# Performance work log

Hardware: AMD Instinct MI355X
Metric: run time of the kernel (lower is better)

The kernel has to match this reference:

```python
import jax, jax.numpy as jnp
import numpy as np

B, H, S, D = 2, 16, 2048, 64
NEG_BIG = -1e12


def setup_inputs() -> dict:
    key = jax.random.key(0)
    k1, k2, k3, k4 = jax.random.split(key, 4)
    query = jax.random.normal(k1, (B, H, S, D), dtype=jnp.float32)
    key_t = jax.random.normal(k2, (B, H, D, S), dtype=jnp.float32)  # pre-transposed key
    value = jax.random.normal(k3, (B, H, S, D), dtype=jnp.float32)
    mask = jax.random.randint(k4, (B, S), 0, 2, dtype=jnp.int32)
    return {"query": query, "key": key_t, "value": value, "mask": mask}


def reference(query, key, value, mask):
    # scores: [B,H,S,S] = query @ key (key already [B,H,D,S]) scaled by 1/sqrt(D)
    scale = 1.0 / np.sqrt(float(query.shape[-1]))
    scores = jnp.einsum('bhsd,bhdt->bhst', query, key) * scale
    # additive mask along the QUERY dimension, broadcast over keys: (B,1,S,1)
    addr = ((1.0 - mask.astype(scores.dtype)) * NEG_BIG).reshape(query.shape[0], 1, query.shape[2], 1)
    scores = scores + addr
    p_attn = jax.nn.softmax(scores, axis=-1)
    return jnp.einsum('bhst,bhtd->bhsd', p_attn, value)
```

## Files before the change

### kernel.cpp

```cpp
#include <hip/hip_runtime.h>
#include <hip/hip_bf16.h>

#define BB 2
#define HH 16
#define SLEN 2048
#define DD 64
#define QB 128
#define KB 64
#define NW 8
#define NT (SLEN / KB)
#define NBH (BB * HH)
#define LOG2E 1.44269504088896340736f

typedef __attribute__((ext_vector_type(8))) short bf16x8;
typedef __attribute__((ext_vector_type(4))) float f32x4;
typedef unsigned short u16;

__device__ __forceinline__ u16 f2bf_rne(float x) {
  union { float f; unsigned u; } v; v.f = x;
  unsigned r = v.u + 0x7fffu + ((v.u >> 16) & 1u);
  return (u16)(r >> 16);
}
__device__ __forceinline__ float bf2f(u16 h) {
  union { float f; unsigned u; } v; v.u = ((unsigned)h) << 16;
  return v.f;
}
__device__ __forceinline__ unsigned cvt_pk_bf16(float lo, float hi) {
  unsigned r;
  asm("v_cvt_pk_bf16_f32 %0, %1, %2" : "=v"(r) : "v"(lo), "v"(hi));
  return r;
}
__device__ __forceinline__ int swz(int row, int col) {
  return row * 64 + (col ^ ((row & 7) << 3));
}
__device__ __forceinline__ void gload_lds16(const u16* g, u16* l) {
  __builtin_amdgcn_global_load_lds(
      (const __attribute__((address_space(1))) unsigned int*)g,
      (__attribute__((address_space(3))) unsigned int*)l, 16, 0, 0);
}

__global__ __launch_bounds__(256) void conv_k(const float* __restrict__ k,
                                              u16* __restrict__ wsKhi,
                                              u16* __restrict__ wsKlo) {
  const int wv = blockIdx.x * 4 + (threadIdx.x >> 6);
  const int l = threadIdx.x & 63;
  const int bh = wv >> 5;
  const int t = (wv & 31) * 64 + l;
  const float* kb = k + (size_t)bh * DD * SLEN;
  u16* oh = wsKhi + ((size_t)bh * SLEN + t) * DD;
  u16* ol = wsKlo + ((size_t)bh * SLEN + t) * DD;
  const int sw = (t & 7) << 3;
#pragma unroll
  for (int g = 0; g < 8; ++g) {
    const int d0 = g * 8;
    bf16x8 hv, lv;
#pragma unroll
    for (int j = 0; j < 8; ++j) {
      float x = kb[(size_t)(d0 + j) * SLEN + t];
      u16 hi = (u16)(__float_as_uint(x) >> 16);
      hv[j] = (short)hi;
      lv[j] = (short)(u16)(__float_as_uint(x - bf2f(hi)) >> 16);
    }
    *reinterpret_cast<bf16x8*>(&oh[d0 ^ sw]) = hv;
    *reinterpret_cast<bf16x8*>(&ol[d0 ^ sw]) = lv;
  }
}

__global__ __launch_bounds__(256) void conv_v(const float* __restrict__ v,
                                              u16* __restrict__ wsVT) {
  const int wv = blockIdx.x * 4 + (threadIdx.x >> 6);
  const int l = threadIdx.x & 63;
  const int bh = wv >> 5;
  const int kt = wv & 31;
  const float* vb = v + ((size_t)bh * SLEN + (size_t)kt * KB) * DD;
  u16* ov = wsVT + (((size_t)bh * NT + kt) * KB + l) * DD;
  const int sw = (l & 7) << 3;
#pragma unroll
  for (int g = 0; g < 8; ++g) {
    const int t0l = g * 8;
    bf16x8 vv;
#pragma unroll
    for (int j = 0; j < 8; ++j)
      vv[j] = (short)f2bf_rne(vb[(size_t)(t0l + j) * DD + l]);
    *reinterpret_cast<bf16x8*>(&ov[t0l ^ sw]) = vv;
  }
}

__global__ __launch_bounds__(512) void attn_fwd_pre(
    const float* __restrict__ q, const u16* __restrict__ wsKhi,
    const u16* __restrict__ wsKlo, const u16* __restrict__ wsVT,
    const int* __restrict__ mask, float* __restrict__ out) {
  __shared__ u16 KhiL[2][KB * DD];
  __shared__ u16 KloL[2][KB * DD];
  __shared__ u16 VTL[2][DD * KB];
  __shared__ u16 Pl[NW][16 * KB];

  const int tid = threadIdx.x;
  const int w = tid >> 6, l = tid & 63, lg = l >> 4, ln = l & 15;

  const int bid = blockIdx.x;
  const int sbid = (bid & 7) * 64 + (bid >> 3);
  const int qt = sbid & 15;
  const int bh = sbid >> 4;
  const int b = bh / HH;

  const float* qbase = q + ((size_t)bh * SLEN + (size_t)qt * QB) * DD;
  const u16* gKhi = wsKhi + (size_t)bh * SLEN * DD;
  const u16* gKlo = wsKlo + (size_t)bh * SLEN * DD;
  const u16* gVT = wsVT + (size_t)bh * NT * (KB * DD);
  float* obase = out + ((size_t)bh * SLEN + (size_t)qt * QB) * DD;

  const int co = tid * 8;

  auto issue = [&](int kt, int buf) {
    gload_lds16(gKhi + kt * (KB * DD) + co, &KhiL[buf][w * 512]);
    gload_lds16(gKlo + kt * (KB * DD) + co, &KloL[buf][w * 512]);
    gload_lds16(gVT + kt * (KB * DD) + co, &VTL[buf][w * 512]);
  };

  issue(0, 0);

  bf16x8 qhi[2], qlo[2];
  {
    const float* qrow = qbase + (size_t)(w * 16 + ln) * DD;
#pragma unroll
    for (int c = 0; c < 2; ++c) {
      int d0 = c * 32 + lg * 8;
#pragma unroll
      for (int j = 0; j < 8; ++j) {
        float x = qrow[d0 + j];
        u16 hi = f2bf_rne(x);
        qhi[c][j] = (short)hi;
        qlo[c][j] = (short)f2bf_rne(x - bf2f(hi));
      }
    }
  }

  const float addv =
      mask[b * SLEN + qt * QB + w * 16 + ln] ? 0.0f : -1e12f * LOG2E;
  const float SC = 0.125f * LOG2E;

  f32x4 oacc[4];
#pragma unroll
  for (int nt = 0; nt < 4; ++nt) oacc[nt] = (f32x4){0.f, 0.f, 0.f, 0.f};
  float mrun = -INFINITY, lrun = 0.f;

  int cur = 0;
  for (int kt = 0; kt < NT; ++kt) {
    if (kt + 1 < NT) {
      issue(kt + 1, cur ^ 1);
      asm volatile("s_waitcnt vmcnt(3)" ::: "memory");
    } else {
      asm volatile("s_waitcnt vmcnt(0)" ::: "memory");
    }
    __builtin_amdgcn_s_barrier();

    f32x4 sacc[4];
#pragma unroll
    for (int nt = 0; nt < 4; ++nt) sacc[nt] = (f32x4){0.f, 0.f, 0.f, 0.f};
    __builtin_amdgcn_s_setprio(1);
#pragma unroll
    for (int c = 0; c < 2; ++c) {
      int d0 = c * 32 + lg * 8;
#pragma unroll
      for (int nt = 0; nt < 4; ++nt) {
        bf16x8 bhf =
            *reinterpret_cast<bf16x8*>(&KhiL[cur][swz(nt * 16 + ln, d0)]);
        bf16x8 blf =
            *reinterpret_cast<bf16x8*>(&KloL[cur][swz(nt * 16 + ln, d0)]);
        sacc[nt] = __builtin_amdgcn_mfma_f32_16x16x32_bf16(bhf, qhi[c], sacc[nt], 0, 0, 0);
        sacc[nt] = __builtin_amdgcn_mfma_f32_16x16x32_bf16(bhf, qlo[c], sacc[nt], 0, 0, 0);
        sacc[nt] = __builtin_amdgcn_mfma_f32_16x16x32_bf16(blf, qhi[c], sacc[nt], 0, 0, 0);
      }
    }
    __builtin_amdgcn_s_setprio(0);

    float sv[4][4];
    float rm = -INFINITY;
#pragma unroll
    for (int nt = 0; nt < 4; ++nt)
#pragma unroll
      for (int r = 0; r < 4; ++r) {
        float x = sacc[nt][r] * SC + addv;
        sv[nt][r] = x;
        rm = fmaxf(rm, x);
      }
    rm = fmaxf(rm, __shfl_xor(rm, 16, 64));
    rm = fmaxf(rm, __shfl_xor(rm, 32, 64));
    float mnew = fmaxf(mrun, rm);
    float sf = exp2f(mrun - mnew);
    mrun = mnew;
    float rs = 0.f;
#pragma unroll
    for (int nt = 0; nt < 4; ++nt)
#pragma unroll
      for (int r = 0; r < 4; ++r) {
        float p = exp2f(sv[nt][r] - mnew);
        sv[nt][r] = p;
        rs += p;
      }
    rs += __shfl_xor(rs, 16, 64);
    rs += __shfl_xor(rs, 32, 64);
    lrun = lrun * sf + rs;
    float sfb[4];
#pragma unroll
    for (int r = 0; r < 4; ++r)
      sfb[r] = __shfl(sf, (l & 48) | (lg * 4 + r), 64);
#pragma unroll
    for (int nt = 0; nt < 4; ++nt)
#pragma unroll
      for (int r = 0; r < 4; ++r) oacc[nt][r] *= sfb[r];

#pragma unroll
    for (int nt = 0; nt < 4; ++nt) {
      uint2 pw;
      pw.x = cvt_pk_bf16(sv[nt][0], sv[nt][1]);
      pw.y = cvt_pk_bf16(sv[nt][2], sv[nt][3]);
      *reinterpret_cast<uint2*>(&Pl[w][swz(ln, nt * 16 + lg * 4)]) = pw;
    }

    __builtin_amdgcn_s_setprio(1);
#pragma unroll
    for (int c = 0; c < 2; ++c) {
      int tc = c * 32 + lg * 8;
      bf16x8 pa = *reinterpret_cast<bf16x8*>(&Pl[w][swz(ln, tc)]);
#pragma unroll
      for (int nt = 0; nt < 4; ++nt) {
        bf16x8 vb =
            *reinterpret_cast<bf16x8*>(&VTL[cur][swz(nt * 16 + ln, tc)]);
        oacc[nt] = __builtin_amdgcn_mfma_f32_16x16x32_bf16(pa, vb, oacc[nt], 0, 0, 0);
      }
    }
    __builtin_amdgcn_s_setprio(0);

    __builtin_amdgcn_s_barrier();
    cur ^= 1;
  }

  float lr[4];
#pragma unroll
  for (int r = 0; r < 4; ++r)
    lr[r] = __shfl(lrun, (l & 48) | (lg * 4 + r), 64);
#pragma unroll
  for (int nt = 0; nt < 4; ++nt)
#pragma unroll
    for (int r = 0; r < 4; ++r) {
      obase[(size_t)(w * 16 + lg * 4 + r) * DD + nt * 16 + ln] =
          oacc[nt][r] / lr[r];
    }
}

__global__ __launch_bounds__(512) void attn_fwd_fb(
    const float* __restrict__ q, const float* __restrict__ k,
    const float* __restrict__ v, const int* __restrict__ mask,
    float* __restrict__ out) {
  __shared__ u16 Khi[KB * DD];
  __shared__ u16 Klo[KB * DD];
  __shared__ u16 VT[DD * KB];
  __shared__ u16 Pl[NW][16 * KB];

  const int tid = threadIdx.x;
  const int w = tid >> 6, l = tid & 63, lg = l >> 4, ln = l & 15;
  const int qt = blockIdx.x;
  const int bh = blockIdx.y;
  const int b = bh / HH;

  const float* qbase = q + ((size_t)bh * SLEN + (size_t)qt * QB) * DD;
  const float* kbase = k + (size_t)bh * DD * SLEN;
  const float* vbase = v + (size_t)bh * SLEN * DD;
  float* obase = out + ((size_t)bh * SLEN + (size_t)qt * QB) * DD;

  const int st_t = tid & 63;
  const int st_d0 = (tid >> 6) * 8;
  const int sv_d = tid & 63;
  const int sv_t0 = (tid >> 6) * 8;

  bf16x8 qhi[2], qlo[2];
  {
    const float* qrow = qbase + (size_t)(w * 16 + ln) * DD;
#pragma unroll
    for (int c = 0; c < 2; ++c) {
      int d0 = c * 32 + lg * 8;
#pragma unroll
      for (int j = 0; j < 8; ++j) {
        float x = qrow[d0 + j];
        u16 hi = f2bf_rne(x);
        qhi[c][j] = (short)hi;
        qlo[c][j] = (short)f2bf_rne(x - bf2f(hi));
      }
    }
  }
  const float addv =
      mask[b * SLEN + qt * QB + w * 16 + ln] ? 0.0f : -1e12f * LOG2E;
  const float SC = 0.125f * LOG2E;

  f32x4 oacc[4];
#pragma unroll
  for (int nt = 0; nt < 4; ++nt) oacc[nt] = (f32x4){0.f, 0.f, 0.f, 0.f};
  float mrun = -INFINITY, lrun = 0.f;

  for (int kt = 0; kt < NT; ++kt) {
    const int t0 = kt * KB;
    __syncthreads();
    bf16x8 khiv, klov, vv;
#pragma unroll
    for (int j = 0; j < 8; ++j) {
      float x = kbase[(size_t)(st_d0 + j) * SLEN + t0 + st_t];
      u16 hi = (u16)(__float_as_uint(x) >> 16);
      khiv[j] = (short)hi;
      klov[j] = (short)(u16)(__float_as_uint(x - bf2f(hi)) >> 16);
    }
#pragma unroll
    for (int j = 0; j < 8; ++j)
      vv[j] = (short)f2bf_rne(vbase[(size_t)(t0 + sv_t0 + j) * DD + sv_d]);
    *reinterpret_cast<bf16x8*>(&Khi[swz(st_t, st_d0)]) = khiv;
    *reinterpret_cast<bf16x8*>(&Klo[swz(st_t, st_d0)]) = klov;
    *reinterpret_cast<bf16x8*>(&VT[swz(sv_d, sv_t0)]) = vv;
    __syncthreads();

    f32x4 sacc[4];
#pragma unroll
    for (int nt = 0; nt < 4; ++nt) sacc[nt] = (f32x4){0.f, 0.f, 0.f, 0.f};
#pragma unroll
    for (int c = 0; c < 2; ++c) {
      int d0 = c * 32 + lg * 8;
#pragma unroll
      for (int nt = 0; nt < 4; ++nt) {
        bf16x8 bhf = *reinterpret_cast<bf16x8*>(&Khi[swz(nt * 16 + ln, d0)]);
        bf16x8 blf = *reinterpret_cast<bf16x8*>(&Klo[swz(nt * 16 + ln, d0)]);
        sacc[nt] = __builtin_amdgcn_mfma_f32_16x16x32_bf16(bhf, qhi[c], sacc[nt], 0, 0, 0);
        sacc[nt] = __builtin_amdgcn_mfma_f32_16x16x32_bf16(bhf, qlo[c], sacc[nt], 0, 0, 0);
        sacc[nt] = __builtin_amdgcn_mfma_f32_16x16x32_bf16(blf, qhi[c], sacc[nt], 0, 0, 0);
      }
    }
    float sv[4][4];
    float rm = -INFINITY;
#pragma unroll
    for (int nt = 0; nt < 4; ++nt)
#pragma unroll
      for (int r = 0; r < 4; ++r) {
        float x = sacc[nt][r] * SC + addv;
        sv[nt][r] = x;
        rm = fmaxf(rm, x);
      }
    rm = fmaxf(rm, __shfl_xor(rm, 16, 64));
    rm = fmaxf(rm, __shfl_xor(rm, 32, 64));
    float mnew = fmaxf(mrun, rm);
    float sf = exp2f(mrun - mnew);
    mrun = mnew;
    float rs = 0.f;
#pragma unroll
    for (int nt = 0; nt < 4; ++nt)
#pragma unroll
      for (int r = 0; r < 4; ++r) {
        float p = exp2f(sv[nt][r] - mnew);
        sv[nt][r] = p;
        rs += p;
      }
    rs += __shfl_xor(rs, 16, 64);
    rs += __shfl_xor(rs, 32, 64);
    lrun = lrun * sf + rs;
    float sfb[4];
#pragma unroll
    for (int r = 0; r < 4; ++r)
      sfb[r] = __shfl(sf, (l & 48) | (lg * 4 + r), 64);
#pragma unroll
    for (int nt = 0; nt < 4; ++nt)
#pragma unroll
      for (int r = 0; r < 4; ++r) oacc[nt][r] *= sfb[r];
#pragma unroll
    for (int nt = 0; nt < 4; ++nt) {
      uint2 pw;
      pw.x = cvt_pk_bf16(sv[nt][0], sv[nt][1]);
      pw.y = cvt_pk_bf16(sv[nt][2], sv[nt][3]);
      *reinterpret_cast<uint2*>(&Pl[w][swz(ln, nt * 16 + lg * 4)]) = pw;
    }
#pragma unroll
    for (int c = 0; c < 2; ++c) {
      int tc = c * 32 + lg * 8;
      bf16x8 pa = *reinterpret_cast<bf16x8*>(&Pl[w][swz(ln, tc)]);
#pragma unroll
      for (int nt = 0; nt < 4; ++nt) {
        bf16x8 vb = *reinterpret_cast<bf16x8*>(&VT[swz(nt * 16 + ln, tc)]);
        oacc[nt] = __builtin_amdgcn_mfma_f32_16x16x32_bf16(pa, vb, oacc[nt], 0, 0, 0);
      }
    }
  }
  float lr[4];
#pragma unroll
  for (int r = 0; r < 4; ++r)
    lr[r] = __shfl(lrun, (l & 48) | (lg * 4 + r), 64);
#pragma unroll
  for (int nt = 0; nt < 4; ++nt)
#pragma unroll
    for (int r = 0; r < 4; ++r) {
      obase[(size_t)(w * 16 + lg * 4 + r) * DD + nt * 16 + ln] =
          oacc[nt][r] / lr[r];
    }
}

extern "C" void kernel_launch(void* const* d_in, const int* in_sizes, int n_in,
                              void* d_out, int out_size, void* d_ws, size_t ws_size,
                              hipStream_t stream) {
  const float* q = (const float*)d_in[0];
  const float* k = (const float*)d_in[1];
  const float* v = (const float*)d_in[2];
  const int* mask = (const int*)d_in[3];
  float* out = (float*)d_out;

  const size_t nKV = (size_t)NBH * SLEN * DD;
  const size_t need = 3 * nKV * sizeof(u16);
  if (ws_size >= need) {
    u16* wsKhi = (u16*)d_ws;
    u16* wsKlo = wsKhi + nKV;
    u16* wsVT = wsKlo + nKV;
    conv_k<<<256, 256, 0, stream>>>(k, wsKhi, wsKlo);
    conv_v<<<256, 256, 0, stream>>>(v, wsVT);
    attn_fwd_pre<<<512, 512, 0, stream>>>(q, wsKhi, wsKlo, wsVT, mask, out);
  } else {
    attn_fwd_fb<<<dim3(SLEN / QB, NBH), 512, 0, stream>>>(q, k, v, mask, out);
  }
}
```

Baseline: 188.6 us.

## Merge K/V conversion kernels with finer split and add lazy softmax rescaling

```diff
diff --git a/kernel.cpp b/kernel.cpp
--- a/kernel.cpp
+++ b/kernel.cpp
@@ -39,50 +39,43 @@
       (__attribute__((address_space(3))) unsigned int*)l, 16, 0, 0);
 }
 
-__global__ __launch_bounds__(256) void conv_k(const float* __restrict__ k,
-                                              u16* __restrict__ wsKhi,
-                                              u16* __restrict__ wsKlo) {
+__global__ __launch_bounds__(256) void conv_kv(const float* __restrict__ k,
+                                               const float* __restrict__ v,
+                                               u16* __restrict__ wsKhi,
+                                               u16* __restrict__ wsKlo,
+                                               u16* __restrict__ wsVT) {
   const int wv = blockIdx.x * 4 + (threadIdx.x >> 6);
   const int l = threadIdx.x & 63;
-  const int bh = wv >> 5;
-  const int t = (wv & 31) * 64 + l;
-  const float* kb = k + (size_t)bh * DD * SLEN;
-  u16* oh = wsKhi + ((size_t)bh * SLEN + t) * DD;
-  u16* ol = wsKlo + ((size_t)bh * SLEN + t) * DD;
-  const int sw = (t & 7) << 3;
-#pragma unroll
-  for (int g = 0; g < 8; ++g) {
-    const int d0 = g * 8;
+  if (wv < 8192) {
+    const int bh = wv >> 8;
+    const int tc = (wv >> 3) & 31;
+    const int g = wv & 7;
+    const int t = tc * 64 + l;
+    const float* kb = k + ((size_t)bh * DD + g * 8) * SLEN + t;
     bf16x8 hv, lv;
 #pragma unroll
     for (int j = 0; j < 8; ++j) {
-      float x = kb[(size_t)(d0 + j) * SLEN + t];
+      float x = kb[(size_t)j * SLEN];
       u16 hi = (u16)(__float_as_uint(x) >> 16);
       hv[j] = (short)hi;
       lv[j] = (short)(u16)(__float_as_uint(x - bf2f(hi)) >> 16);
     }
-    *reinterpret_cast<bf16x8*>(&oh[d0 ^ sw]) = hv;
-    *reinterpret_cast<bf16x8*>(&ol[d0 ^ sw]) = lv;
-  }
-}
-
-__global__ __launch_bounds__(256) void conv_v(const float* __restrict__ v,
-                                              u16* __restrict__ wsVT) {
-  const int wv = blockIdx.x * 4 + (threadIdx.x >> 6);
-  const int l = threadIdx.x & 63;
-  const int bh = wv >> 5;
-  const int kt = wv & 31;
-  const float* vb = v + ((size_t)bh * SLEN + (size_t)kt * KB) * DD;
-  u16* ov = wsVT + (((size_t)bh * NT + kt) * KB + l) * DD;
-  const int sw = (l & 7) << 3;
-#pragma unroll
-  for (int g = 0; g < 8; ++g) {
-    const int t0l = g * 8;
+    const size_t o = ((size_t)bh * SLEN + t) * DD + ((g * 8) ^ ((t & 7) << 3));
+    *reinterpret_cast<bf16x8*>(&wsKhi[o]) = hv;
+    *reinterpret_cast<bf16x8*>(&wsKlo[o]) = lv;
+  } else {
+    const int wv2 = wv - 8192;
+    const int bh = wv2 >> 8;
+    const int kt = (wv2 >> 3) & 31;
+    const int g = wv2 & 7;
+    const float* vb = v + ((size_t)bh * SLEN + (size_t)kt * KB + g * 8) * DD + l;
     bf16x8 vv;
 #pragma unroll
     for (int j = 0; j < 8; ++j)
-      vv[j] = (short)f2bf_rne(vb[(size_t)(t0l + j) * DD + l]);
-    *reinterpret_cast<bf16x8*>(&ov[t0l ^ sw]) = vv;
+      vv[j] = (short)f2bf_rne(vb[(size_t)j * DD]);
+    const size_t o = (((size_t)bh * NT + kt) * KB + l) * DD +
+                     ((g * 8) ^ ((l & 7) << 3));
+    *reinterpret_cast<bf16x8*>(&wsVT[o]) = vv;
   }
 }
 
@@ -176,40 +169,43 @@
     __builtin_amdgcn_s_setprio(0);
 
     float sv[4][4];
-    float rm = -INFINITY;
 #pragma unroll
     for (int nt = 0; nt < 4; ++nt)
 #pragma unroll
-      for (int r = 0; r < 4; ++r) {
-        float x = sacc[nt][r] * SC + addv;
-        sv[nt][r] = x;
-        rm = fmaxf(rm, x);
-      }
+      for (int r = 0; r < 4; ++r) sv[nt][r] = sacc[nt][r] * SC + addv;
+    float a0 = fmaxf(fmaxf(sv[0][0], sv[0][1]), fmaxf(sv[0][2], sv[0][3]));
+    float a1 = fmaxf(fmaxf(sv[1][0], sv[1][1]), fmaxf(sv[1][2], sv[1][3]));
+    float a2 = fmaxf(fmaxf(sv[2][0], sv[2][1]), fmaxf(sv[2][2], sv[2][3]));
+    float a3 = fmaxf(fmaxf(sv[3][0], sv[3][1]), fmaxf(sv[3][2], sv[3][3]));
+    float rm = fmaxf(fmaxf(a0, a1), fmaxf(a2, a3));
     rm = fmaxf(rm, __shfl_xor(rm, 16, 64));
     rm = fmaxf(rm, __shfl_xor(rm, 32, 64));
-    float mnew = fmaxf(mrun, rm);
-    float sf = exp2f(mrun - mnew);
-    mrun = mnew;
+    if (!__all(rm <= mrun + 8.f)) {
+      float mnew = fmaxf(mrun, rm);
+      float sf = exp2f(mrun - mnew);
+      mrun = mnew;
+      float sfb[4];
+#pragma unroll
+      for (int r = 0; r < 4; ++r)
+        sfb[r] = __shfl(sf, (l & 48) | (lg * 4 + r), 64);
+      lrun *= sf;
+#pragma unroll
+      for (int nt = 0; nt < 4; ++nt)
+#pragma unroll
+        for (int r = 0; r < 4; ++r) oacc[nt][r] *= sfb[r];
+    }
     float rs = 0.f;
 #pragma unroll
     for (int nt = 0; nt < 4; ++nt)
 #pragma unroll
       for (int r = 0; r < 4; ++r) {
-        float p = exp2f(sv[nt][r] - mnew);
+        float p = exp2f(sv[nt][r] - mrun);
         sv[nt][r] = p;
         rs += p;
       }
     rs += __shfl_xor(rs, 16, 64);
     rs += __shfl_xor(rs, 32, 64);
-    lrun = lrun * sf + rs;
-    float sfb[4];
-#pragma unroll
-    for (int r = 0; r < 4; ++r)
-      sfb[r] = __shfl(sf, (l & 48) | (lg * 4 + r), 64);
-#pragma unroll
-    for (int nt = 0; nt < 4; ++nt)
-#pragma unroll
-      for (int r = 0; r < 4; ++r) oacc[nt][r] *= sfb[r];
+    lrun += rs;
 
 #pragma unroll
     for (int nt = 0; nt < 4; ++nt) {
@@ -414,8 +410,7 @@
     u16* wsKhi = (u16*)d_ws;
     u16* wsKlo = wsKhi + nKV;
     u16* wsVT = wsKlo + nKV;
-    conv_k<<<256, 256, 0, stream>>>(k, wsKhi, wsKlo);
-    conv_v<<<256, 256, 0, stream>>>(v, wsVT);
+    conv_kv<<<4096, 256, 0, stream>>>(k, v, wsKhi, wsKlo, wsVT);
     attn_fwd_pre<<<512, 512, 0, stream>>>(q, wsKhi, wsKlo, wsVT, mask, out);
   } else {
     attn_fwd_fb<<<dim3(SLEN / QB, NBH), 512, 0, stream>>>(q, k, v, mask, out);
```

Measured after the change: 180.9 us. 4.1% less time.
